# Kernel optimization log

Hardware: AMD Instinct MI355X
Metric: run time of the kernel (lower is better)

The kernel has to match this reference:

```python
import jax, jax.numpy as jnp
import numpy as np

B, T_ENC, T_DEC = 64, 512, 400
IN_DIM, R = 80, 2
D_ENC, D_ATT, D_PRE = 256, 256, 128
NEG_INF = -1e9


def _gru(x, h, Wi, Wh, bi, bh):
    # PyTorch GRUCell math
    gi = x @ Wi + bi
    gh = h @ Wh + bh
    ir, iz, inn = jnp.split(gi, 3, axis=-1)
    hr, hz, hn = jnp.split(gh, 3, axis=-1)
    r = jax.nn.sigmoid(ir + hr)
    z = jax.nn.sigmoid(iz + hz)
    n = jnp.tanh(inn + r * hn)
    return (1.0 - z) * n + z * h


def setup_inputs() -> dict:
    key = jax.random.key(0)
    ks = jax.random.split(key, 32)
    s = 0.05
    d_in = IN_DIM * R
    inp = {
        "encoder_outputs": jax.random.normal(ks[0], (B, T_ENC, D_ENC), jnp.float32),
        "inputs": jax.random.normal(ks[1], (B, T_DEC, d_in), jnp.float32),
        "memory_lengths": jax.random.randint(ks[2], (B,), T_ENC // 2, T_ENC + 1).astype(jnp.int32),
        # prenet
        "pre_W1": s * jax.random.normal(ks[3], (d_in, 256), jnp.float32),
        "pre_b1": jnp.zeros((256,), jnp.float32),
        "pre_W2": s * jax.random.normal(ks[4], (256, 128), jnp.float32),
        "pre_b2": jnp.zeros((128,), jnp.float32),
        # Bahdanau attention
        "mem_W": s * jax.random.normal(ks[5], (D_ENC, D_ATT), jnp.float32),
        "q_W": s * jax.random.normal(ks[6], (256, D_ATT), jnp.float32),
        "v_W": s * jax.random.normal(ks[7], (D_ATT, 1), jnp.float32),
        # attention GRUCell: input = cat(prenet 128, attention 256) = 384
        "att_Wi": s * jax.random.normal(ks[8], (384, 768), jnp.float32),
        "att_Wh": s * jax.random.normal(ks[9], (256, 768), jnp.float32),
        "att_bi": jnp.zeros((768,), jnp.float32),
        "att_bh": jnp.zeros((768,), jnp.float32),
        # project_to_decoder_in
        "proj_in_W": s * jax.random.normal(ks[10], (512, 256), jnp.float32),
        "proj_in_b": jnp.zeros((256,), jnp.float32),
        # decoder GRUCells
        "dec1_Wi": s * jax.random.normal(ks[11], (256, 768), jnp.float32),
        "dec1_Wh": s * jax.random.normal(ks[12], (256, 768), jnp.float32),
        "dec1_bi": jnp.zeros((768,), jnp.float32),
        "dec1_bh": jnp.zeros((768,), jnp.float32),
        "dec2_Wi": s * jax.random.normal(ks[13], (256, 768), jnp.float32),
        "dec2_Wh": s * jax.random.normal(ks[14], (256, 768), jnp.float32),
        "dec2_bi": jnp.zeros((768,), jnp.float32),
        "dec2_bh": jnp.zeros((768,), jnp.float32),
        # output projections
        "mel_W": s * jax.random.normal(ks[15], (256, d_in), jnp.float32),
        "mel_b": jnp.zeros((d_in,), jnp.float32),
        "gate_W": s * jax.random.normal(ks[16], (256, R), jnp.float32),
        "gate_b": jnp.zeros((R,), jnp.float32),
    }
    return inp


def _decoder_forward(encoder_outputs, inputs, memory_lengths,
                     pre_W1, pre_b1, pre_W2, pre_b2,
                     mem_W, q_W, v_W,
                     att_Wi, att_Wh, att_bi, att_bh,
                     proj_in_W, proj_in_b,
                     dec1_Wi, dec1_Wh, dec1_bi, dec1_bh,
                     dec2_Wi, dec2_Wh, dec2_bi, dec2_bh,
                     mel_W, mel_b, gate_W, gate_b):
    Bq, Tq, _ = encoder_outputs.shape
    processed_memory = encoder_outputs @ mem_W  # (B, T_enc, D_att)
    valid = jnp.arange(Tq)[None, :] < memory_lengths[:, None]  # (B, T_enc)

    # teacher forcing: input at step t is inputs[t-1], zeros at t=0
    prev = jnp.concatenate([jnp.zeros_like(inputs[:, :1]), inputs[:, :-1]], axis=1)
    prev = jnp.swapaxes(prev, 0, 1)  # (T_dec, B, in_dim*r)

    def prenet(x):
        # dropout is identity in eval mode
        h = jax.nn.relu(x @ pre_W1 + pre_b1)
        return jax.nn.relu(h @ pre_W2 + pre_b2)

    def step(carry, x_prev):
        att_h, h1, h2, cur_att = carry
        pre = prenet(x_prev)  # (B, 128)
        cell_in = jnp.concatenate([pre, cur_att], axis=-1)  # (B, 384)
        att_h = _gru(cell_in, att_h, att_Wi, att_Wh, att_bi, att_bh)  # (B, 256)
        # Bahdanau alignment over encoder memory
        score = jnp.squeeze(
            jnp.tanh(processed_memory + (att_h @ q_W)[:, None, :]) @ v_W, -1)  # (B, T_enc)
        score = jnp.where(valid, score, NEG_INF)
        align = jax.nn.softmax(score, axis=-1)
        cur_att = jnp.einsum('bt,btd->bd', align, encoder_outputs)  # (B, 256)
        dec_in = jnp.concatenate([att_h, cur_att], axis=-1) @ proj_in_W + proj_in_b
        h1 = _gru(dec_in, h1, dec1_Wi, dec1_Wh, dec1_bi, dec1_bh)
        d = h1 + dec_in
        h2 = _gru(d, h2, dec2_Wi, dec2_Wh, dec2_bi, dec2_bh)
        d = h2 + d
        gate = jax.nn.sigmoid(d @ gate_W + gate_b)  # (B, r)
        out = d @ mel_W + mel_b  # (B, in_dim*r)
        return (att_h, h1, h2, cur_att), (out, align, gate)

    z = jnp.zeros((Bq, 256), encoder_outputs.dtype)
    init = (z, z, z, z)
    _, (outs, aligns, gates) = jax.lax.scan(step, init, prev)
    outputs = jnp.swapaxes(outs, 0, 1)      # (B, T_dec, in_dim*r)
    alignments = jnp.swapaxes(aligns, 0, 1)  # (B, T_dec, T_enc)
    gates = jnp.swapaxes(gates, 0, 1)        # (B, T_dec, r)
    return outputs, alignments, gates


def reference(encoder_outputs, inputs, memory_lengths,
              pre_W1, pre_b1, pre_W2, pre_b2,
              mem_W, q_W, v_W,
              att_Wi, att_Wh, att_bi, att_bh,
              proj_in_W, proj_in_b,
              dec1_Wi, dec1_Wh, dec1_bi, dec1_bh,
              dec2_Wi, dec2_Wh, dec2_bi, dec2_bh,
              mel_W, mel_b, gate_W, gate_b):
    return _decoder_forward(encoder_outputs, inputs, memory_lengths,
                            pre_W1, pre_b1, pre_W2, pre_b2,
                            mem_W, q_W, v_W,
                            att_Wi, att_Wh, att_bi, att_bh,
                            proj_in_W, proj_in_b,
                            dec1_Wi, dec1_Wh, dec1_bi, dec1_bh,
                            dec2_Wi, dec2_Wh, dec2_bi, dec2_bh,
                            mel_W, mel_b, gate_W, gate_b)
```

## Files before the change

kernel.cpp:

```cpp
#include <hip/hip_runtime.h>

#define TDEC 400
#define NTH 512
#define NWG 256

typedef float f32x4 __attribute__((ext_vector_type(4)));
typedef unsigned u32x4 __attribute__((ext_vector_type(4)));
typedef unsigned u32x2 __attribute__((ext_vector_type(2)));

#define OFF_BAR   0
#define OFF_ATTH  11264
#define OFF_H1    44032
#define OFF_H2    76800
#define OFF_CURP  109568
#define OFF_ATTS  125952
#define OFF_Q     126208
#define ZERO_FLOATS 142592
#define OFF_D1    142592
#define OFF_SUMS  158976
#define OFF_C1    184576
#define OFF_PRE   185600
#define OFF_PMB   1824000
#define OFF_ENCB  6018304
#define OFF_D2A   10212608
#define T_WIT_A   10212608
#define T_WHT_A   10507520
#define T_M1T     10704128
#define T_WHT1    11097344
#define T_PJT     11293952
#define T_WIT2    11425024
#define T_WHT2    11621632
#define T_QWT     11818240
#define T_M1      11883776
#define OFF_BLOB  16766208

#define BLOB_N   26112
#define BLOB_STR 26624
#define BO_AI  0
#define BO_AH  4608
#define BO_Q   7680
#define BO_M1  8704
#define BO_H1  14848
#define BO_PJ  17920
#define BO_I2  19968
#define BO_H2  23040

#define AOFF 4096000
#define GOFF 17203200

#define MSTI  (8*1024)
#define GENI  (9*1024)
#define FAILI (10*1024)

__device__ __forceinline__ float fsig(float x){ return 1.0f/(1.0f+__expf(-x)); }
__device__ __forceinline__ float ftanh(float x){ float e = __expf(2.0f*x); return 1.0f - 2.0f/(e+1.0f); }
__device__ __forceinline__ float blo(unsigned u){ return __uint_as_float(u<<16); }
__device__ __forceinline__ float bhi(unsigned u){ return __uint_as_float(u & 0xffff0000u); }

__device__ __forceinline__ f32x4 cload16(const float* p){
  f32x4 r;
  asm volatile("global_load_dwordx4 %0, %1, off sc0 sc1" : "=v"(r) : "v"(p));
  return r;
}
__device__ __forceinline__ f32x4 cload16w(const float* p){
  f32x4 r;
  asm volatile("global_load_dwordx4 %0, %1, off sc0 sc1\n\ts_waitcnt vmcnt(0)" : "=v"(r) : "v"(p));
  return r;
}
__device__ __forceinline__ u32x4 cload16u(const unsigned short* p){
  u32x4 r;
  asm volatile("global_load_dwordx4 %0, %1, off sc0 sc1" : "=v"(r) : "v"(p));
  return r;
}
__device__ __forceinline__ float aload4(const float* p){
  unsigned u = __hip_atomic_load((const unsigned*)p, __ATOMIC_RELAXED, __HIP_MEMORY_SCOPE_AGENT);
  return __uint_as_float(u);
}
__device__ __forceinline__ void astore4(float* p, float v){
  __hip_atomic_store((unsigned*)p, __float_as_uint(v), __ATOMIC_RELAXED, __HIP_MEMORY_SCOPE_AGENT);
}
__device__ __forceinline__ void aadd(float* p, float v){
  __hip_atomic_fetch_add(p, v, __ATOMIC_RELAXED, __HIP_MEMORY_SCOPE_AGENT);
}
__device__ __forceinline__ int aloadi(const int* p){
  return __hip_atomic_load(p, __ATOMIC_RELAXED, __HIP_MEMORY_SCOPE_AGENT);
}

__device__ __forceinline__ void ldsbar(){
  __builtin_amdgcn_sched_barrier(0);
  asm volatile("s_waitcnt lgkmcnt(0)" ::: "memory");
  __builtin_amdgcn_s_barrier();
  __builtin_amdgcn_sched_barrier(0);
}

__device__ __forceinline__ void gbar(int* bar, int g, int l, int n){
  asm volatile("s_waitcnt vmcnt(0)" ::: "memory");
  __syncthreads();
  if (threadIdx.x == 0){
    if (aloadi(&bar[FAILI]) == 0){
      int a = __hip_atomic_fetch_add(&bar[(l&7)*1024 + g*64], 1, __ATOMIC_RELAXED, __HIP_MEMORY_SCOPE_AGENT);
      if (a == 8*n - 1){
        int m = __hip_atomic_fetch_add(&bar[MSTI + g*64], 1, __ATOMIC_RELAXED, __HIP_MEMORY_SCOPE_AGENT);
        if (m == 8*n - 1)
          __hip_atomic_store(&bar[GENI + g*64], n, __ATOMIC_RELAXED, __HIP_MEMORY_SCOPE_AGENT);
      }
      int sp = 0;
      while (aloadi(&bar[GENI + g*64]) < n){
        __builtin_amdgcn_s_sleep(1);
        if (++sp > (1<<20)){
          __hip_atomic_store(&bar[FAILI], 1, __ATOMIC_RELAXED, __HIP_MEMORY_SCOPE_AGENT);
          break;
        }
      }
    }
  }
  __syncthreads();
}

__device__ __forceinline__ unsigned short f2bf(float f){
  unsigned u = __float_as_uint(f);
  return (unsigned short)((u + 0x7fffu + ((u>>16)&1u)) >> 16);
}

template<int N8>
__device__ __forceinline__ float bdot(const unsigned short* wr, const float* xr){
  f32x4 accA = 0.f, accB = 0.f;
  #pragma unroll 4
  for (int k = 0; k < N8; ++k){
    u32x4 u = *(const u32x4*)(wr + k*8);
    f32x4 a = *(const f32x4*)(xr + k*8);
    f32x4 b = *(const f32x4*)(xr + k*8 + 4);
    f32x4 w0, w1;
    w0[0]=blo(u[0]); w0[1]=bhi(u[0]); w0[2]=blo(u[1]); w0[3]=bhi(u[1]);
    w1[0]=blo(u[2]); w1[1]=bhi(u[2]); w1[2]=blo(u[3]); w1[3]=bhi(u[3]);
    accA += w0*a; accB += w1*b;
  }
  f32x4 s = accA + accB;
  return s[0]+s[1]+s[2]+s[3];
}

__global__ __launch_bounds__(256, 1) void transpose_k(const float* __restrict__ in,
                                                      float* __restrict__ outp, int K, int C){
  __shared__ float tl[32][33];
  int c0 = blockIdx.x * 32, k0 = blockIdx.y * 32;
  int tx = threadIdx.x & 31, ty = threadIdx.x >> 5;
  for (int i = ty; i < 32; i += 8){
    int k = k0 + i, c = c0 + tx;
    if (k < K && c < C) tl[i][tx] = in[k * C + c];
  }
  __syncthreads();
  for (int i = ty; i < 32; i += 8){
    int c = c0 + i, k = k0 + tx;
    if (c < C && k < K) outp[c * K + k] = tl[tx][i];
  }
}

__global__ __launch_bounds__(128, 1) void fuse_k(const float* __restrict__ projW,
    const float* __restrict__ d1Wi, float* __restrict__ M1){
  int jt = blockIdx.x % 6, i = blockIdx.x / 6;
  int j = jt * 128 + threadIdx.x;
  float acc = 0.f;
  for (int k = 0; k < 256; ++k) acc += projW[i*256+k] * d1Wi[k*768+j];
  M1[i*768+j] = acc;
}

__global__ __launch_bounds__(256, 1) void c1_k(const float* __restrict__ projB,
    const float* __restrict__ d1Wi, const float* __restrict__ d1Bi, float* __restrict__ C1){
  int j = blockIdx.x * 256 + threadIdx.x;
  float acc = d1Bi[j];
  for (int k = 0; k < 256; ++k) acc += projB[k] * d1Wi[k*768+j];
  C1[j] = acc;
}

__global__ __launch_bounds__(512, 1) void pack_k(float* __restrict__ ws){
  int sl = blockIdx.x;
  const float* TAI = ws + T_WIT_A;
  const float* TAH = ws + T_WHT_A;
  const float* TM1 = ws + T_M1T;
  const float* TH1 = ws + T_WHT1;
  const float* TPJ = ws + T_PJT;
  const float* TI2 = ws + T_WIT2;
  const float* TH2 = ws + T_WHT2;
  const float* TQ  = ws + T_QWT;
  unsigned short* blob = (unsigned short*)(ws + OFF_BLOB) + (size_t)sl * BLOB_STR;
  for (int idx = threadIdx.x; idx < BLOB_N; idx += 512){
    float v; int cs, k, o;
    if (idx < BO_AH){ cs = idx / 384; k = idx - cs*384;
      v = TAI[((cs%3)*256 + sl*4 + cs/3)*384 + k]; }
    else if (idx < BO_Q){ o = idx - BO_AH; cs = o >> 8; k = o & 255;
      v = TAH[((cs%3)*256 + sl*4 + cs/3)*256 + k]; }
    else if (idx < BO_M1){ o = idx - BO_Q; cs = o >> 8; k = o & 255;
      v = TQ[(sl*4 + cs)*256 + k]; }
    else if (idx < BO_H1){ o = idx - BO_M1; cs = o >> 9; k = o & 511;
      v = TM1[((cs%3)*256 + sl*4 + cs/3)*512 + k]; }
    else if (idx < BO_PJ){ o = idx - BO_H1; cs = o >> 8; k = o & 255;
      v = TH1[((cs%3)*256 + sl*4 + cs/3)*256 + k]; }
    else if (idx < BO_I2){ o = idx - BO_PJ; cs = o >> 9; k = o & 511;
      v = TPJ[(sl*4 + cs)*512 + k]; }
    else if (idx < BO_H2){ o = idx - BO_I2; cs = o >> 8; k = o & 255;
      v = TI2[((cs%3)*256 + sl*4 + cs/3)*256 + k]; }
    else { o = idx - BO_H2; cs = o >> 8; k = o & 255;
      v = TH2[((cs%3)*256 + sl*4 + cs/3)*256 + k]; }
    blob[idx] = f2bf(v);
  }
}

__global__ __launch_bounds__(256, 1) void qt_k(const float* __restrict__ ws,
                                               float* __restrict__ out){
  unsigned short* qtb = (unsigned short*)(out + GOFF);
  const float* TQ = ws + T_QWT;
  int idx = blockIdx.x * 256 + threadIdx.x;
  int it = idx >> 11, j = (idx >> 3) & 255, e = idx & 7;
  qtb[idx] = f2bf(TQ[j*256 + it*8 + e]);
}

__global__ __launch_bounds__(NTH, 1) void prenet_k(float* __restrict__ ws,
    const float* __restrict__ inp, const float* __restrict__ W1, const float* __restrict__ B1,
    const float* __restrict__ W2, const float* __restrict__ B2){
  __shared__ float xT[160 * 33];
  __shared__ float hT[256 * 33];
  int t = blockIdx.x, half = blockIdx.y, tid = threadIdx.x;
  int bbase = half * 32;
  for (int r = tid; r < 32 * 160; r += NTH){
    int b2 = r / 160; int k = r - b2 * 160;
    xT[k * 33 + b2] = (t == 0) ? 0.f : inp[((bbase + b2) * TDEC + (t - 1)) * 160 + k];
  }
  __syncthreads();
  int bl = tid & 31, slot = tid >> 5;
  float acc1[16];
  #pragma unroll
  for (int i = 0; i < 16; ++i) acc1[i] = 0.f;
  for (int k = 0; k < 160; ++k){
    float xv = xT[k * 33 + bl];
    const float* wr = W1 + k * 256 + slot * 16;
    #pragma unroll
    for (int i = 0; i < 16; ++i) acc1[i] += xv * wr[i];
  }
  #pragma unroll
  for (int i = 0; i < 16; ++i){
    int c = slot * 16 + i;
    hT[c * 33 + bl] = fmaxf(acc1[i] + B1[c], 0.f);
  }
  __syncthreads();
  float acc2[8];
  #pragma unroll
  for (int i = 0; i < 8; ++i) acc2[i] = 0.f;
  for (int k = 0; k < 256; ++k){
    float hv = hT[k * 33 + bl];
    const float* wr = W2 + k * 128 + slot * 8;
    #pragma unroll
    for (int i = 0; i < 8; ++i) acc2[i] += hv * wr[i];
  }
  unsigned short* dst = (unsigned short*)(ws + OFF_PRE) + (size_t)t*8192 + (bbase + bl)*128 + slot*8;
  u32x4 pk;
  #pragma unroll
  for (int i = 0; i < 4; ++i){
    float v0 = fmaxf(acc2[2*i] + B2[slot*8 + 2*i], 0.f);
    float v1 = fmaxf(acc2[2*i+1] + B2[slot*8 + 2*i+1], 0.f);
    pk[i] = (unsigned)f2bf(v0) | ((unsigned)f2bf(v1) << 16);
  }
  *(u32x4*)dst = pk;
}

__global__ __launch_bounds__(NTH, 1) void pm_k(float* __restrict__ ws,
    const float* __restrict__ enc, const float* __restrict__ memW){
  int wg = blockIdx.x, tid = threadIdx.x;
  int b = wg & 63, th = wg >> 6;
  int slot = tid & 7, tt = tid >> 3;
  int trow = th * 64 + tt;
  const float* er = enc + ((size_t)(b * 512 + trow)) * 256;
  f32x4 acc[8];
  #pragma unroll
  for (int i = 0; i < 8; ++i) acc[i] = 0.f;
  for (int k = 0; k < 256; ++k){
    float ev = er[k];
    const f32x4* wr = (const f32x4*)(memW + k * 256 + slot * 32);
    #pragma unroll
    for (int i = 0; i < 8; ++i) acc[i] += ev * wr[i];
  }
  unsigned short* pmB = (unsigned short*)(ws + OFF_PMB);
  unsigned short* dst = pmB + ((size_t)(b * 512 + trow)) * 256 + slot * 32;
  #pragma unroll
  for (int i = 0; i < 8; ++i){
    u32x2 pk;
    pk[0] = (unsigned)f2bf(acc[i][0]) | ((unsigned)f2bf(acc[i][1]) << 16);
    pk[1] = (unsigned)f2bf(acc[i][2]) | ((unsigned)f2bf(acc[i][3]) << 16);
    *(u32x2*)(dst + i * 4) = pk;
  }
  const float* e2 = enc + ((size_t)(b * 512 + th * 64)) * 256;
  unsigned* eb = (unsigned*)((unsigned short*)(ws + OFF_ENCB) + ((size_t)(b * 512 + th * 64)) * 256);
  for (int i = tid; i < 64 * 128; i += NTH){
    float v0 = e2[i * 2], v1 = e2[i * 2 + 1];
    eb[i] = (unsigned)f2bf(v0) | ((unsigned)f2bf(v1) << 16);
  }
}

__global__ __launch_bounds__(NTH, 2) void decoder_k(
    float* __restrict__ ws, float* __restrict__ out,
    const int* __restrict__ memlen,
    const float* __restrict__ vW,
    const float* __restrict__ attBi, const float* __restrict__ attBh,
    const float* __restrict__ projB,
    const float* __restrict__ d1Bh,
    const float* __restrict__ d2Bi, const float* __restrict__ d2Bh)
{
  const int wg = blockIdx.x, tid = threadIdx.x;
  int* bar = (int*)ws;
  float* attH = ws + OFF_ATTH;
  float* h1a  = ws + OFF_H1;
  float* h2a  = ws + OFF_H2;
  float* const curB[2]  = { ws + OFF_CURP, ws + OFF_Q };
  float* const attSB[2] = { ws + OFF_ATTS, ws + OFF_ATTS + 64 };
  float* d1v  = ws + OFF_D1;
  const float* C1v = ws + OFF_C1;
  const unsigned short* preB16 = (const unsigned short*)(ws + OFF_PRE);
  const unsigned short* pmB  = (const unsigned short*)(ws + OFF_PMB);
  const unsigned short* encB = (const unsigned short*)(ws + OFF_ENCB);
  const unsigned short* qtb = (const unsigned short*)(out + GOFF);
  float* d2a  = ws + OFF_D2A;

  __shared__ float BUF[12416];
  __shared__ float qL[256], vL[256];
  __shared__ float eL[128];
  __shared__ float red[512];
  __shared__ float ewGi[192], ewGh[192], pdec[128];

  if (tid < 256) vL[tid] = vW[tid];

  const int g = wg >> 6, l = wg & 63;
  const int sl = l;
  const int b0 = g << 4;
  const int b2 = b0 + (l >> 2), ch2 = l & 3;
  const int len2 = memlen[b2];
  const unsigned short* blob = (const unsigned short*)(ws + OFF_BLOB) + (size_t)sl * BLOB_STR;

  const int bq = tid & 15, x = tid >> 4;
  const int cs = (x >= 12) ? (x - 12) : x;
  const int gg = cs % 3, jh = cs / 3;
  const int col = gg * 256 + sl * 4 + jh;

  const int r0 = tid >> 6, c0 = (tid & 63) << 2;
  const int r1 = r0 + 8;
  const int prr = tid >> 4, pcc = (tid & 15) * 8;

  u32x4 pmv[8], env[8];
  {
    int te = tid >> 2, part = tid & 3;
    const u32x4* pmp = (const u32x4*)(pmB + ((size_t)(b2*512 + ch2*128 + te))*256 + part*64);
    #pragma unroll
    for (int i = 0; i < 8; ++i) pmv[i] = pmp[i];
    int ich = tid >> 5, dblk = tid & 31;
    const unsigned short* ep = encB + ((size_t)(b2*512 + ch2*128 + ich*8))*256 + dblk*8;
    #pragma unroll
    for (int i = 0; i < 8; ++i) env[i] = *(const u32x4*)(ep + i*256);
  }

  f32x4 pH0, pH1, pC0, pC1;
  float pS0, pS1;
  u32x4 ppre = 0u;
  {
    const float* gHn = attH + 16384 + b0*256;
    const float* gCn = curB[1] + b0*256;
    pH0 = cload16(gHn + (r0<<8) + c0); pH1 = cload16(gHn + (r1<<8) + c0);
    pC0 = cload16(gCn + (r0<<8) + c0); pC1 = cload16(gCn + (r1<<8) + c0);
    pS0 = aload4(attSB[1] + b0 + r0);  pS1 = aload4(attSB[1] + b0 + r1);
    if (tid < 256) ppre = cload16u(preB16 + (b0 + prr)*128 + pcc);
  }

  int bn = 0;
  for (int t = 0; t < TDEC; ++t){
    const int w = t & 1, rb = w ^ 1;

    {
      float* xL = BUF;
      float* hL = BUF + 6208;
      asm volatile("s_waitcnt vmcnt(0)" : "+v"(pH0),"+v"(pH1),"+v"(pC0),"+v"(pC1),"+v"(ppre));
      float iv0 = pS0 > 0.f ? 1.f/pS0 : 0.f, iv1 = pS1 > 0.f ? 1.f/pS1 : 0.f;
      if (tid < 256){
        float* xd = xL + prr*388 + pcc;
        xd[0]=blo(ppre[0]); xd[1]=bhi(ppre[0]); xd[2]=blo(ppre[1]); xd[3]=bhi(ppre[1]);
        xd[4]=blo(ppre[2]); xd[5]=bhi(ppre[2]); xd[6]=blo(ppre[3]); xd[7]=bhi(ppre[3]);
      }
      *(f32x4*)(hL + r0*260 + c0) = pH0; *(f32x4*)(hL + r1*260 + c0) = pH1;
      *(f32x4*)(xL + r0*388 + 128 + c0) = pC0*iv0; *(f32x4*)(xL + r1*388 + 128 + c0) = pC1*iv1;
      if (tid < 64) astore4(curB[w] + wg*64 + tid, 0.f);
      if (sl == 0 && tid < 16) astore4(attSB[w] + b0 + tid, 0.f);
      ldsbar();
      if (x < 12)
        ewGi[cs*16 + bq] = bdot<48>(blob + BO_AI + cs*384, xL + bq*388) + attBi[col];
      else if (x < 24)
        ewGh[cs*16 + bq] = bdot<32>(blob + BO_AH + cs*256, hL + bq*260) + attBh[col];
      ldsbar();
      if (tid < 64){
        int bt = tid & 15, jj = tid >> 4;
        int j = sl*4 + jj;
        float ir = ewGi[(jj*3+0)*16+bt] + ewGh[(jj*3+0)*16+bt];
        float iz = ewGi[(jj*3+1)*16+bt] + ewGh[(jj*3+1)*16+bt];
        float inn = ewGi[(jj*3+2)*16+bt];
        float hn  = ewGh[(jj*3+2)*16+bt];
        float rg = fsig(ir), z = fsig(iz);
        float n = ftanh(inn + rg * hn);
        float h = hL[bt*260 + j];
        astore4(attH + w*16384 + (b0+bt)*256 + j, (1.f - z)*n + z*h);
      }
    }
    gbar(bar, g, l, ++bn);

    {
      float* ctxP = BUF;
      float* qIn  = BUF + 8192;
      if (tid < 64){
        f32x4 v = cload16w(attH + w*16384 + b2*256 + tid*4);
        *(f32x4*)(qIn + tid*4) = v;
      }
      ldsbar();
      {
        int j = tid & 255, hf = tid >> 8;
        const unsigned short* qw = qtb + j*8 + (size_t)hf*16*2048;
        const float* qx = qIn + hf*128;
        f32x4 aA = 0.f, aB = 0.f;
        #pragma unroll 4
        for (int it = 0; it < 16; ++it){
          u32x4 u = *(const u32x4*)(qw + (size_t)it*2048);
          f32x4 a = *(const f32x4*)(qx + it*8);
          f32x4 b = *(const f32x4*)(qx + it*8 + 4);
          f32x4 w0, w1;
          w0[0]=blo(u[0]); w0[1]=bhi(u[0]); w0[2]=blo(u[1]); w0[3]=bhi(u[1]);
          w1[0]=blo(u[2]); w1[1]=bhi(u[2]); w1[2]=blo(u[3]); w1[3]=bhi(u[3]);
          aA += w0*a; aB += w1*b;
        }
        f32x4 s4 = aA + aB;
        red[tid] = s4[0]+s4[1]+s4[2]+s4[3];
      }
      ldsbar();
      if (tid < 256) qL[tid] = red[tid] + red[tid + 256];
      ldsbar();
      {
        int te = tid >> 2, part = tid & 3;
        int ge = ch2*128 + te;
        float a4 = 0.f;
        #pragma unroll
        for (int i = 0; i < 8; ++i){
          u32x4 u = pmv[i];
          int kb = part*64 + i*8;
          a4 += ftanh(blo(u[0]) + qL[kb+0]) * vL[kb+0];
          a4 += ftanh(bhi(u[0]) + qL[kb+1]) * vL[kb+1];
          a4 += ftanh(blo(u[1]) + qL[kb+2]) * vL[kb+2];
          a4 += ftanh(bhi(u[1]) + qL[kb+3]) * vL[kb+3];
          a4 += ftanh(blo(u[2]) + qL[kb+4]) * vL[kb+4];
          a4 += ftanh(bhi(u[2]) + qL[kb+5]) * vL[kb+5];
          a4 += ftanh(blo(u[3]) + qL[kb+6]) * vL[kb+6];
          a4 += ftanh(bhi(u[3]) + qL[kb+7]) * vL[kb+7];
        }
        a4 += __shfl_xor(a4, 1);
        a4 += __shfl_xor(a4, 2);
        float e = (ge < len2) ? __expf(a4) : 0.f;
        if (part == 0){
          eL[te] = e;
          out[AOFF + ((size_t)(b2*TDEC + t))*512 + ge] = e;
        }
      }
      ldsbar();
      if (tid < 64){
        float s = eL[tid] + eL[tid + 64];
        #pragma unroll
        for (int o = 32; o > 0; o >>= 1) s += __shfl_down(s, o);
        if (tid == 0) aadd(attSB[w] + b2, s);
      }
      {
        int ich = tid >> 5, dblk = tid & 31;
        f32x4 acA = 0.f, acB = 0.f;
        #pragma unroll
        for (int i = 0; i < 8; ++i){
          u32x4 u = env[i];
          float e = eL[ich*8 + i];
          acA[0] += e*blo(u[0]); acA[1] += e*bhi(u[0]);
          acA[2] += e*blo(u[1]); acA[3] += e*bhi(u[1]);
          acB[0] += e*blo(u[2]); acB[1] += e*bhi(u[2]);
          acB[2] += e*blo(u[3]); acB[3] += e*bhi(u[3]);
        }
        *(f32x4*)(ctxP + tid*8) = acA;
        *(f32x4*)(ctxP + tid*8 + 4) = acB;
      }
      ldsbar();
      if (tid < 256){
        int dblk = tid >> 3, d = tid & 7;
        float s = 0.f;
        #pragma unroll
        for (int i = 0; i < 16; ++i) s += ctxP[i*256 + dblk*8 + d];
        aadd(curB[w] + b2*256 + dblk*8 + d, s);
      }
    }
    gbar(bar, g, l, ++bn);

    {
      float* yL  = BUF;
      float* h1L = BUF + 8256;
      const float* gA = attH + w*16384 + b0*256;
      const float* gH = h1a + rb*16384 + b0*256;
      const float* gC = curB[w] + b0*256;
      f32x4 vA0 = cload16(gA + (r0<<8) + c0), vA1 = cload16(gA + (r1<<8) + c0);
      f32x4 vH0 = cload16(gH + (r0<<8) + c0), vH1 = cload16(gH + (r1<<8) + c0);
      f32x4 vC0 = cload16(gC + (r0<<8) + c0), vC1 = cload16(gC + (r1<<8) + c0);
      float s0 = aload4(attSB[w] + b0 + r0), s1 = aload4(attSB[w] + b0 + r1);
      asm volatile("s_waitcnt vmcnt(0)" : "+v"(vA0),"+v"(vA1),"+v"(vH0),"+v"(vH1),"+v"(vC0),"+v"(vC1));
      float iv0 = s0 > 0.f ? 1.f/s0 : 0.f, iv1 = s1 > 0.f ? 1.f/s1 : 0.f;
      *(f32x4*)(yL + r0*516 + c0) = vA0;       *(f32x4*)(yL + r1*516 + c0) = vA1;
      *(f32x4*)(h1L + r0*260 + c0) = vH0;      *(f32x4*)(h1L + r1*260 + c0) = vH1;
      *(f32x4*)(yL + r0*516 + 256 + c0) = vC0*iv0; *(f32x4*)(yL + r1*516 + 256 + c0) = vC1*iv1;
      ldsbar();
      if (x < 12)
        ewGi[cs*16 + bq] = bdot<64>(blob + BO_M1 + cs*512, yL + bq*516) + C1v[col];
      else if (x < 24)
        ewGh[cs*16 + bq] = bdot<32>(blob + BO_H1 + cs*256, h1L + bq*260) + d1Bh[col];
      else {
        int idx = tid - 384;
        int bq2 = idx & 15, cc = (idx >> 4) & 3, half = idx >> 6;
        pdec[idx] = bdot<32>(blob + BO_PJ + cc*512 + half*256, yL + bq2*516 + half*256);
      }
      ldsbar();
      if (tid < 64){
        int bt = tid & 15, jj = tid >> 4;
        int j = sl*4 + jj;
        float ir = ewGi[(jj*3+0)*16+bt] + ewGh[(jj*3+0)*16+bt];
        float iz = ewGi[(jj*3+1)*16+bt] + ewGh[(jj*3+1)*16+bt];
        float inn = ewGi[(jj*3+2)*16+bt];
        float hn  = ewGh[(jj*3+2)*16+bt];
        float rg = fsig(ir), z = fsig(iz);
        float n = ftanh(inn + rg * hn);
        float hv = h1L[bt*260 + j];
        float hnew = (1.f - z)*n + z*hv;
        float dec = pdec[jj*16 + bt] + pdec[64 + jj*16 + bt] + projB[j];
        astore4(h1a + w*16384 + (b0+bt)*256 + j, hnew);
        astore4(d1v + (b0+bt)*256 + j, hnew + dec);
      }
      if (sl == 0 && tid < 16)
        ws[OFF_SUMS + t*64 + b0 + tid] = aload4(attSB[w] + b0 + tid);
    }
    gbar(bar, g, l, ++bn);

    {
      float* dL  = BUF;
      float* h2L = BUF + 4160;
      const float* gD = d1v + b0*256;
      const float* gH = h2a + rb*16384 + b0*256;
      f32x4 vD0 = cload16(gD + (r0<<8) + c0), vD1 = cload16(gD + (r1<<8) + c0);
      f32x4 vH0 = cload16(gH + (r0<<8) + c0), vH1 = cload16(gH + (r1<<8) + c0);
      asm volatile("s_waitcnt vmcnt(0)" : "+v"(vD0),"+v"(vD1),"+v"(vH0),"+v"(vH1));
      {
        const float* gHn = attH + w*16384 + b0*256;
        const float* gCn = curB[w] + b0*256;
        pH0 = cload16(gHn + (r0<<8) + c0); pH1 = cload16(gHn + (r1<<8) + c0);
        pC0 = cload16(gCn + (r0<<8) + c0); pC1 = cload16(gCn + (r1<<8) + c0);
        pS0 = aload4(attSB[w] + b0 + r0);  pS1 = aload4(attSB[w] + b0 + r1);
        int tn = (t + 1 < TDEC) ? (t + 1) : 0;
        if (tid < 256) ppre = cload16u(preB16 + (size_t)tn*8192 + (b0 + prr)*128 + pcc);
      }
      *(f32x4*)(dL + r0*260 + c0) = vD0;  *(f32x4*)(dL + r1*260 + c0) = vD1;
      *(f32x4*)(h2L + r0*260 + c0) = vH0; *(f32x4*)(h2L + r1*260 + c0) = vH1;
      ldsbar();
      if (x < 12)
        ewGi[cs*16 + bq] = bdot<32>(blob + BO_I2 + cs*256, dL + bq*260) + d2Bi[col];
      else if (x < 24)
        ewGh[cs*16 + bq] = bdot<32>(blob + BO_H2 + cs*256, h2L + bq*260) + d2Bh[col];
      ldsbar();
      if (tid < 64){
        int bt = tid & 15, jj = tid >> 4;
        int j = sl*4 + jj;
        float ir = ewGi[(jj*3+0)*16+bt] + ewGh[(jj*3+0)*16+bt];
        float iz = ewGi[(jj*3+1)*16+bt] + ewGh[(jj*3+1)*16+bt];
        float inn = ewGi[(jj*3+2)*16+bt];
        float hn  = ewGh[(jj*3+2)*16+bt];
        float rg = fsig(ir), z = fsig(iz);
        float n = ftanh(inn + rg * hn);
        float hv = h2L[bt*260 + j];
        float hnew = (1.f - z)*n + z*hv;
        astore4(h2a + w*16384 + (b0+bt)*256 + j, hnew);
        d2a[t*16384 + j*64 + (b0+bt)] = hnew + dL[bt*260 + j];
      }
      ldsbar();
    }
  }
}

__global__ __launch_bounds__(NTH, 1) void rescale_k(const float* __restrict__ ws,
                                                    float* __restrict__ out){
  int blk = blockIdx.x;
  int b = blk / TDEC, t = blk - b * TDEC;
  float s = ws[OFF_SUMS + t*64 + b];
  float inv = (s > 0.f) ? 1.f/s : 0.f;
  out[AOFF + (size_t)blk*512 + threadIdx.x] *= inv;
}

__global__ __launch_bounds__(NTH, 1) void outproj_k(const float* __restrict__ ws,
    float* __restrict__ out, const float* __restrict__ melW, const float* __restrict__ melB,
    const float* __restrict__ gateW, const float* __restrict__ gateB){
  int t = blockIdx.x, tid = threadIdx.x;
  int cx = tid & 255, bh = tid >> 8;
  const float* src = ws + OFF_D2A + t*16384 + bh*32;
  float acc[32];
  #pragma unroll
  for (int i = 0; i < 32; ++i) acc[i] = 0.f;
  bool ismel = (cx < 160);
  bool isgate = (cx >= 160 && cx < 162);
  for (int j = 0; j < 256; ++j){
    float wv = 0.f;
    if (ismel) wv = melW[j*160 + cx];
    else if (isgate) wv = gateW[j*2 + (cx - 160)];
    const f32x4* dp = (const f32x4*)(src + j*64);
    f32x4 vv[8];
    #pragma unroll
    for (int q = 0; q < 8; ++q) vv[q] = dp[q];
    #pragma unroll
    for (int q = 0; q < 8; ++q){
      acc[q*4+0] += vv[q][0]*wv; acc[q*4+1] += vv[q][1]*wv;
      acc[q*4+2] += vv[q][2]*wv; acc[q*4+3] += vv[q][3]*wv;
    }
  }
  if (ismel){
    float bb = melB[cx];
    #pragma unroll
    for (int i = 0; i < 32; ++i){
      int b = bh*32 + i;
      out[((size_t)(b*TDEC + t))*160 + cx] = acc[i] + bb;
    }
  } else if (isgate){
    int g = cx - 160;
    float bb = gateB[g];
    #pragma unroll
    for (int i = 0; i < 32; ++i){
      int b = bh*32 + i;
      out[GOFF + ((size_t)(b*TDEC + t))*2 + g] = fsig(acc[i] + bb);
    }
  }
}

extern "C" void kernel_launch(void* const* d_in, const int* in_sizes, int n_in,
                              void* d_out, int out_size, void* d_ws, size_t ws_size,
                              hipStream_t stream)
{
  (void)in_sizes; (void)n_in; (void)out_size; (void)ws_size;
  const float* enc   = (const float*)d_in[0];
  const float* inp   = (const float*)d_in[1];
  const int*   mlen  = (const int*)d_in[2];
  const float* preW1 = (const float*)d_in[3];
  const float* preB1 = (const float*)d_in[4];
  const float* preW2 = (const float*)d_in[5];
  const float* preB2 = (const float*)d_in[6];
  const float* memW  = (const float*)d_in[7];
  const float* qW    = (const float*)d_in[8];
  const float* vW    = (const float*)d_in[9];
  const float* attWi = (const float*)d_in[10];
  const float* attWh = (const float*)d_in[11];
  const float* attBi = (const float*)d_in[12];
  const float* attBh = (const float*)d_in[13];
  const float* projW = (const float*)d_in[14];
  const float* projB = (const float*)d_in[15];
  const float* d1Wi  = (const float*)d_in[16];
  const float* d1Wh  = (const float*)d_in[17];
  const float* d1Bi  = (const float*)d_in[18];
  const float* d1Bh  = (const float*)d_in[19];
  const float* d2Wi  = (const float*)d_in[20];
  const float* d2Wh  = (const float*)d_in[21];
  const float* d2Bi  = (const float*)d_in[22];
  const float* d2Bh  = (const float*)d_in[23];
  const float* melW  = (const float*)d_in[24];
  const float* melB  = (const float*)d_in[25];
  const float* gateW = (const float*)d_in[26];
  const float* gateB = (const float*)d_in[27];
  float* ws = (float*)d_ws;
  float* out = (float*)d_out;

  hipMemsetAsync(d_ws, 0, (size_t)ZERO_FLOATS * sizeof(float), stream);

  dim3 tt(256);
  transpose_k<<<dim3(24, 12), tt, 0, stream>>>(attWi, ws + T_WIT_A, 384, 768);
  transpose_k<<<dim3(24, 8),  tt, 0, stream>>>(attWh, ws + T_WHT_A, 256, 768);
  transpose_k<<<dim3(24, 8),  tt, 0, stream>>>(d1Wh,  ws + T_WHT1, 256, 768);
  transpose_k<<<dim3(24, 8),  tt, 0, stream>>>(d2Wi,  ws + T_WIT2, 256, 768);
  transpose_k<<<dim3(24, 8),  tt, 0, stream>>>(d2Wh,  ws + T_WHT2, 256, 768);
  transpose_k<<<dim3(8, 16),  tt, 0, stream>>>(projW, ws + T_PJT, 512, 256);
  transpose_k<<<dim3(8, 8),   tt, 0, stream>>>(qW,    ws + T_QWT, 256, 256);
  fuse_k<<<3072, 128, 0, stream>>>(projW, d1Wi, ws + T_M1);
  c1_k<<<3, 256, 0, stream>>>(projB, d1Wi, d1Bi, ws + OFF_C1);
  transpose_k<<<dim3(24, 16), tt, 0, stream>>>(ws + T_M1, ws + T_M1T, 512, 768);
  pack_k<<<64, NTH, 0, stream>>>(ws);
  qt_k<<<256, 256, 0, stream>>>(ws, out);

  prenet_k<<<dim3(TDEC, 2), NTH, 0, stream>>>(ws, inp, preW1, preB1, preW2, preB2);
  pm_k<<<512, NTH, 0, stream>>>(ws, enc, memW);
  decoder_k<<<NWG, NTH, 0, stream>>>(ws, out, mlen, vW, attBi, attBh, projB,
                                     d1Bh, d2Bi, d2Bh);
  rescale_k<<<64 * TDEC, NTH, 0, stream>>>(ws, out);
  outproj_k<<<TDEC, NTH, 0, stream>>>(ws, out, melW, melB, gateW, gateB);
}
```

Baseline: 13.32 ms.

## Double workgroup count to 512 with 8-batch groups and split-K GRU dots

Grows the persistent decoder grid from 256 to 512 workgroups, so each group of 64 workgroups handles 8 batch rows instead of 16 and each attention chunk covers 64 encoder positions instead of 128. The GRU gate dot products are split across two K halves and combined with a lane shuffle, and GRU biases are hoisted into registers before the time loop. The aim is to shorten the per-step serial work between the grid barriers and use more CUs. In exchange the grid barriers span more workgroups, and the query projection and per-step global loads are duplicated across more workgroups.

```diff
diff --git a/kernel.cpp b/kernel.cpp
--- a/kernel.cpp
+++ b/kernel.cpp
@@ -2,7 +2,7 @@
 
 #define TDEC 400
 #define NTH 512
-#define NWG 256
+#define NWG 512
 
 typedef float f32x4 __attribute__((ext_vector_type(4)));
 typedef unsigned u32x4 __attribute__((ext_vector_type(4)));
@@ -319,52 +319,56 @@
   const unsigned short* qtb = (const unsigned short*)(out + GOFF);
   float* d2a  = ws + OFF_D2A;
 
-  __shared__ float BUF[12416];
+  __shared__ float BUF[6208];
   __shared__ float qL[256], vL[256];
-  __shared__ float eL[128];
-  __shared__ float red[512];
-  __shared__ float ewGi[192], ewGh[192], pdec[128];
+  __shared__ float eL[64];
+  __shared__ float ewGi[96], ewGh[96], pdec[32];
 
   if (tid < 256) vL[tid] = vW[tid];
 
   const int g = wg >> 6, l = wg & 63;
   const int sl = l;
-  const int b0 = g << 4;
-  const int b2 = b0 + (l >> 2), ch2 = l & 3;
+  const int b0 = g << 3;
+  const int b2 = b0 + (l >> 3), ch2 = l & 7;
   const int len2 = memlen[b2];
   const unsigned short* blob = (const unsigned short*)(ws + OFF_BLOB) + (size_t)sl * BLOB_STR;
 
-  const int bq = tid & 15, x = tid >> 4;
-  const int cs = (x >= 12) ? (x - 12) : x;
-  const int gg = cs % 3, jh = cs / 3;
-  const int col = gg * 256 + sl * 4 + jh;
-
+  const int bq = tid & 7, x = tid >> 3;
   const int r0 = tid >> 6, c0 = (tid & 63) << 2;
-  const int r1 = r0 + 8;
   const int prr = tid >> 4, pcc = (tid & 15) * 8;
 
-  u32x4 pmv[8], env[8];
+  int cs = 0, kh = 0;
+  if (x < 24){ cs = x >> 1; kh = x & 1; }
+  else if (x < 48){ cs = (x - 24) >> 1; kh = x & 1; }
+  float rb0 = 0.f, rb1 = 0.f, rb2 = 0.f;
+  if (x < 48 && kh == 0){
+    int gg2 = cs % 3, jh2 = cs / 3;
+    int col = gg2*256 + sl*4 + jh2;
+    if (x < 24){ rb0 = attBi[col]; rb1 = C1v[col];  rb2 = d2Bi[col]; }
+    else       { rb0 = attBh[col]; rb1 = d1Bh[col]; rb2 = d2Bh[col]; }
+  }
+  const float pjB = (tid < 32) ? projB[sl*4 + (tid>>3)] : 0.f;
+
+  u32x4 pmv[4]; u32x2 env2[8];
   {
-    int te = tid >> 2, part = tid & 3;
-    const u32x4* pmp = (const u32x4*)(pmB + ((size_t)(b2*512 + ch2*128 + te))*256 + part*64);
-    #pragma unroll
-    for (int i = 0; i < 8; ++i) pmv[i] = pmp[i];
-    int ich = tid >> 5, dblk = tid & 31;
-    const unsigned short* ep = encB + ((size_t)(b2*512 + ch2*128 + ich*8))*256 + dblk*8;
-    #pragma unroll
-    for (int i = 0; i < 8; ++i) env[i] = *(const u32x4*)(ep + i*256);
-  }
-
-  f32x4 pH0, pH1, pC0, pC1;
-  float pS0, pS1;
+    int te = tid >> 3, part = tid & 7;
+    const u32x4* pmp = (const u32x4*)(pmB + ((size_t)(b2*512 + ch2*64 + te))*256 + part*32);
+    #pragma unroll
+    for (int i = 0; i < 4; ++i) pmv[i] = pmp[i];
+    int ich = tid >> 6, dd = tid & 63;
+    const unsigned short* ep = encB + ((size_t)(b2*512 + ch2*64 + ich*8))*256 + dd*4;
+    #pragma unroll
+    for (int i = 0; i < 8; ++i) env2[i] = *(const u32x2*)(ep + i*256);
+  }
+
+  f32x4 pH, pC;
+  float pS;
   u32x4 ppre = 0u;
   {
-    const float* gHn = attH + 16384 + b0*256;
-    const float* gCn = curB[1] + b0*256;
-    pH0 = cload16(gHn + (r0<<8) + c0); pH1 = cload16(gHn + (r1<<8) + c0);
-    pC0 = cload16(gCn + (r0<<8) + c0); pC1 = cload16(gCn + (r1<<8) + c0);
-    pS0 = aload4(attSB[1] + b0 + r0);  pS1 = aload4(attSB[1] + b0 + r1);
-    if (tid < 256) ppre = cload16u(preB16 + (b0 + prr)*128 + pcc);
+    pH = cload16(attH + 16384 + (b0+r0)*256 + c0);
+    pC = cload16(curB[1] + (b0+r0)*256 + c0);
+    pS = aload4(attSB[1] + b0 + r0);
+    if (tid < 128) ppre = cload16u(preB16 + (b0 + prr)*128 + pcc);
   }
 
   int bn = 0;
@@ -373,31 +377,36 @@
 
     {
       float* xL = BUF;
-      float* hL = BUF + 6208;
-      asm volatile("s_waitcnt vmcnt(0)" : "+v"(pH0),"+v"(pH1),"+v"(pC0),"+v"(pC1),"+v"(ppre));
-      float iv0 = pS0 > 0.f ? 1.f/pS0 : 0.f, iv1 = pS1 > 0.f ? 1.f/pS1 : 0.f;
-      if (tid < 256){
+      float* hL = BUF + 3104;
+      asm volatile("s_waitcnt vmcnt(0)" : "+v"(pH),"+v"(pC),"+v"(ppre));
+      float iv = pS > 0.f ? 1.f/pS : 0.f;
+      if (tid < 128){
         float* xd = xL + prr*388 + pcc;
         xd[0]=blo(ppre[0]); xd[1]=bhi(ppre[0]); xd[2]=blo(ppre[1]); xd[3]=bhi(ppre[1]);
         xd[4]=blo(ppre[2]); xd[5]=bhi(ppre[2]); xd[6]=blo(ppre[3]); xd[7]=bhi(ppre[3]);
       }
-      *(f32x4*)(hL + r0*260 + c0) = pH0; *(f32x4*)(hL + r1*260 + c0) = pH1;
-      *(f32x4*)(xL + r0*388 + 128 + c0) = pC0*iv0; *(f32x4*)(xL + r1*388 + 128 + c0) = pC1*iv1;
-      if (tid < 64) astore4(curB[w] + wg*64 + tid, 0.f);
-      if (sl == 0 && tid < 16) astore4(attSB[w] + b0 + tid, 0.f);
-      ldsbar();
-      if (x < 12)
-        ewGi[cs*16 + bq] = bdot<48>(blob + BO_AI + cs*384, xL + bq*388) + attBi[col];
-      else if (x < 24)
-        ewGh[cs*16 + bq] = bdot<32>(blob + BO_AH + cs*256, hL + bq*260) + attBh[col];
-      ldsbar();
-      if (tid < 64){
-        int bt = tid & 15, jj = tid >> 4;
+      *(f32x4*)(hL + r0*260 + c0) = pH;
+      *(f32x4*)(xL + r0*388 + 128 + c0) = pC*iv;
+      if (tid < 32) astore4(curB[w] + wg*32 + tid, 0.f);
+      if (l == 0 && tid < 8) astore4(attSB[w] + b0 + tid, 0.f);
+      ldsbar();
+      {
+        float acc = 0.f;
+        if (x < 24)       acc = bdot<24>(blob + BO_AI + cs*384 + kh*192, xL + bq*388 + kh*192);
+        else if (x < 48)  acc = bdot<16>(blob + BO_AH + cs*256 + kh*128, hL + bq*260 + kh*128);
+        if (x < 48){
+          acc += __shfl_xor(acc, 8);
+          if (kh == 0) (x < 24 ? ewGi : ewGh)[cs*8 + bq] = acc + rb0;
+        }
+      }
+      ldsbar();
+      if (tid < 32){
+        int bt = tid & 7, jj = tid >> 3;
         int j = sl*4 + jj;
-        float ir = ewGi[(jj*3+0)*16+bt] + ewGh[(jj*3+0)*16+bt];
-        float iz = ewGi[(jj*3+1)*16+bt] + ewGh[(jj*3+1)*16+bt];
-        float inn = ewGi[(jj*3+2)*16+bt];
-        float hn  = ewGh[(jj*3+2)*16+bt];
+        float ir = ewGi[(jj*3+0)*8+bt] + ewGh[(jj*3+0)*8+bt];
+        float iz = ewGi[(jj*3+1)*8+bt] + ewGh[(jj*3+1)*8+bt];
+        float inn = ewGi[(jj*3+2)*8+bt];
+        float hn  = ewGh[(jj*3+2)*8+bt];
         float rg = fsig(ir), z = fsig(iz);
         float n = ftanh(inn + rg * hn);
         float h = hL[bt*260 + j];
@@ -408,41 +417,37 @@
 
     {
       float* ctxP = BUF;
-      float* qIn  = BUF + 8192;
+      float* qIn  = BUF + 2560;
       if (tid < 64){
         f32x4 v = cload16w(attH + w*16384 + b2*256 + tid*4);
         *(f32x4*)(qIn + tid*4) = v;
       }
       ldsbar();
-      {
-        int j = tid & 255, hf = tid >> 8;
-        const unsigned short* qw = qtb + j*8 + (size_t)hf*16*2048;
-        const float* qx = qIn + hf*128;
+      if (tid < 256){
+        const unsigned short* qw = qtb + tid*8;
         f32x4 aA = 0.f, aB = 0.f;
         #pragma unroll 4
-        for (int it = 0; it < 16; ++it){
+        for (int it = 0; it < 32; ++it){
           u32x4 u = *(const u32x4*)(qw + (size_t)it*2048);
-          f32x4 a = *(const f32x4*)(qx + it*8);
-          f32x4 b = *(const f32x4*)(qx + it*8 + 4);
+          f32x4 a = *(const f32x4*)(qIn + it*8);
+          f32x4 b = *(const f32x4*)(qIn + it*8 + 4);
           f32x4 w0, w1;
           w0[0]=blo(u[0]); w0[1]=bhi(u[0]); w0[2]=blo(u[1]); w0[3]=bhi(u[1]);
           w1[0]=blo(u[2]); w1[1]=bhi(u[2]); w1[2]=blo(u[3]); w1[3]=bhi(u[3]);
           aA += w0*a; aB += w1*b;
         }
         f32x4 s4 = aA + aB;
-        red[tid] = s4[0]+s4[1]+s4[2]+s4[3];
-      }
-      ldsbar();
-      if (tid < 256) qL[tid] = red[tid] + red[tid + 256];
+        qL[tid] = s4[0]+s4[1]+s4[2]+s4[3];
+      }
       ldsbar();
       {
-        int te = tid >> 2, part = tid & 3;
-        int ge = ch2*128 + te;
+        int te = tid >> 3, part = tid & 7;
+        int ge = ch2*64 + te;
         float a4 = 0.f;
         #pragma unroll
-        for (int i = 0; i < 8; ++i){
+        for (int i = 0; i < 4; ++i){
           u32x4 u = pmv[i];
-          int kb = part*64 + i*8;
+          int kb = part*32 + i*8;
           a4 += ftanh(blo(u[0]) + qL[kb+0]) * vL[kb+0];
           a4 += ftanh(bhi(u[0]) + qL[kb+1]) * vL[kb+1];
           a4 += ftanh(blo(u[1]) + qL[kb+2]) * vL[kb+2];
@@ -454,6 +459,7 @@
         }
         a4 += __shfl_xor(a4, 1);
         a4 += __shfl_xor(a4, 2);
+        a4 += __shfl_xor(a4, 4);
         float e = (ge < len2) ? __expf(a4) : 0.f;
         if (part == 0){
           eL[te] = e;
@@ -462,115 +468,116 @@
       }
       ldsbar();
       if (tid < 64){
-        float s = eL[tid] + eL[tid + 64];
+        float s = eL[tid];
         #pragma unroll
         for (int o = 32; o > 0; o >>= 1) s += __shfl_down(s, o);
         if (tid == 0) aadd(attSB[w] + b2, s);
       }
       {
-        int ich = tid >> 5, dblk = tid & 31;
-        f32x4 acA = 0.f, acB = 0.f;
+        int ich = tid >> 6, dd = tid & 63;
+        f32x4 ac = 0.f;
         #pragma unroll
         for (int i = 0; i < 8; ++i){
-          u32x4 u = env[i];
+          u32x2 u = env2[i];
           float e = eL[ich*8 + i];
-          acA[0] += e*blo(u[0]); acA[1] += e*bhi(u[0]);
-          acA[2] += e*blo(u[1]); acA[3] += e*bhi(u[1]);
-          acB[0] += e*blo(u[2]); acB[1] += e*bhi(u[2]);
-          acB[2] += e*blo(u[3]); acB[3] += e*bhi(u[3]);
-        }
-        *(f32x4*)(ctxP + tid*8) = acA;
-        *(f32x4*)(ctxP + tid*8 + 4) = acB;
+          ac[0] += e*blo(u[0]); ac[1] += e*bhi(u[0]);
+          ac[2] += e*blo(u[1]); ac[3] += e*bhi(u[1]);
+        }
+        *(f32x4*)(ctxP + ich*256 + dd*4) = ac;
       }
       ldsbar();
       if (tid < 256){
-        int dblk = tid >> 3, d = tid & 7;
         float s = 0.f;
         #pragma unroll
-        for (int i = 0; i < 16; ++i) s += ctxP[i*256 + dblk*8 + d];
-        aadd(curB[w] + b2*256 + dblk*8 + d, s);
+        for (int i = 0; i < 8; ++i) s += ctxP[i*256 + tid];
+        aadd(curB[w] + b2*256 + tid, s);
       }
     }
     gbar(bar, g, l, ++bn);
 
     {
       float* yL  = BUF;
-      float* h1L = BUF + 8256;
-      const float* gA = attH + w*16384 + b0*256;
-      const float* gH = h1a + rb*16384 + b0*256;
-      const float* gC = curB[w] + b0*256;
-      f32x4 vA0 = cload16(gA + (r0<<8) + c0), vA1 = cload16(gA + (r1<<8) + c0);
-      f32x4 vH0 = cload16(gH + (r0<<8) + c0), vH1 = cload16(gH + (r1<<8) + c0);
-      f32x4 vC0 = cload16(gC + (r0<<8) + c0), vC1 = cload16(gC + (r1<<8) + c0);
-      float s0 = aload4(attSB[w] + b0 + r0), s1 = aload4(attSB[w] + b0 + r1);
-      asm volatile("s_waitcnt vmcnt(0)" : "+v"(vA0),"+v"(vA1),"+v"(vH0),"+v"(vH1),"+v"(vC0),"+v"(vC1));
-      float iv0 = s0 > 0.f ? 1.f/s0 : 0.f, iv1 = s1 > 0.f ? 1.f/s1 : 0.f;
-      *(f32x4*)(yL + r0*516 + c0) = vA0;       *(f32x4*)(yL + r1*516 + c0) = vA1;
-      *(f32x4*)(h1L + r0*260 + c0) = vH0;      *(f32x4*)(h1L + r1*260 + c0) = vH1;
-      *(f32x4*)(yL + r0*516 + 256 + c0) = vC0*iv0; *(f32x4*)(yL + r1*516 + 256 + c0) = vC1*iv1;
-      ldsbar();
-      if (x < 12)
-        ewGi[cs*16 + bq] = bdot<64>(blob + BO_M1 + cs*512, yL + bq*516) + C1v[col];
-      else if (x < 24)
-        ewGh[cs*16 + bq] = bdot<32>(blob + BO_H1 + cs*256, h1L + bq*260) + d1Bh[col];
-      else {
-        int idx = tid - 384;
-        int bq2 = idx & 15, cc = (idx >> 4) & 3, half = idx >> 6;
-        pdec[idx] = bdot<32>(blob + BO_PJ + cc*512 + half*256, yL + bq2*516 + half*256);
-      }
-      ldsbar();
-      if (tid < 64){
-        int bt = tid & 15, jj = tid >> 4;
+      float* h1L = BUF + 4128;
+      f32x4 vA = cload16(attH + w*16384 + (b0+r0)*256 + c0);
+      f32x4 vH = cload16(h1a + rb*16384 + (b0+r0)*256 + c0);
+      f32x4 vC = cload16(curB[w] + (b0+r0)*256 + c0);
+      float s0 = aload4(attSB[w] + b0 + r0);
+      asm volatile("s_waitcnt vmcnt(0)" : "+v"(vA),"+v"(vH),"+v"(vC));
+      float iv = s0 > 0.f ? 1.f/s0 : 0.f;
+      *(f32x4*)(yL + r0*516 + c0) = vA;
+      *(f32x4*)(h1L + r0*260 + c0) = vH;
+      *(f32x4*)(yL + r0*516 + 256 + c0) = vC*iv;
+      ldsbar();
+      {
+        float acc = 0.f;
+        if (x < 24)       acc = bdot<32>(blob + BO_M1 + cs*512 + kh*256, yL + bq*516 + kh*256);
+        else if (x < 48)  acc = bdot<16>(blob + BO_H1 + cs*256 + kh*128, h1L + bq*260 + kh*128);
+        else {
+          int idx = x - 48, cc = idx >> 2, qq = idx & 3;
+          acc = bdot<16>(blob + BO_PJ + cc*512 + qq*128, yL + bq*516 + qq*128);
+          acc += __shfl_xor(acc, 8);
+          acc += __shfl_xor(acc, 16);
+          if (qq == 0) pdec[cc*8 + bq] = acc;
+        }
+        if (x < 48){
+          acc += __shfl_xor(acc, 8);
+          if (kh == 0) (x < 24 ? ewGi : ewGh)[cs*8 + bq] = acc + rb1;
+        }
+      }
+      ldsbar();
+      if (tid < 32){
+        int bt = tid & 7, jj = tid >> 3;
         int j = sl*4 + jj;
-        float ir = ewGi[(jj*3+0)*16+bt] + ewGh[(jj*3+0)*16+bt];
-        float iz = ewGi[(jj*3+1)*16+bt] + ewGh[(jj*3+1)*16+bt];
-        float inn = ewGi[(jj*3+2)*16+bt];
-        float hn  = ewGh[(jj*3+2)*16+bt];
+        float ir = ewGi[(jj*3+0)*8+bt] + ewGh[(jj*3+0)*8+bt];
+        float iz = ewGi[(jj*3+1)*8+bt] + ewGh[(jj*3+1)*8+bt];
+        float inn = ewGi[(jj*3+2)*8+bt];
+        float hn  = ewGh[(jj*3+2)*8+bt];
         float rg = fsig(ir), z = fsig(iz);
         float n = ftanh(inn + rg * hn);
         float hv = h1L[bt*260 + j];
         float hnew = (1.f - z)*n + z*hv;
-        float dec = pdec[jj*16 + bt] + pdec[64 + jj*16 + bt] + projB[j];
+        float dec = pdec[jj*8 + bt] + pjB;
         astore4(h1a + w*16384 + (b0+bt)*256 + j, hnew);
         astore4(d1v + (b0+bt)*256 + j, hnew + dec);
       }
-      if (sl == 0 && tid < 16)
+      if (l == 0 && tid < 8)
         ws[OFF_SUMS + t*64 + b0 + tid] = aload4(attSB[w] + b0 + tid);
     }
     gbar(bar, g, l, ++bn);
 
     {
       float* dL  = BUF;
-      float* h2L = BUF + 4160;
-      const float* gD = d1v + b0*256;
-      const float* gH = h2a + rb*16384 + b0*256;
-      f32x4 vD0 = cload16(gD + (r0<<8) + c0), vD1 = cload16(gD + (r1<<8) + c0);
-      f32x4 vH0 = cload16(gH + (r0<<8) + c0), vH1 = cload16(gH + (r1<<8) + c0);
-      asm volatile("s_waitcnt vmcnt(0)" : "+v"(vD0),"+v"(vD1),"+v"(vH0),"+v"(vH1));
+      float* h2L = BUF + 2080;
+      f32x4 vD = cload16(d1v + (b0+r0)*256 + c0);
+      f32x4 vH = cload16(h2a + rb*16384 + (b0+r0)*256 + c0);
+      asm volatile("s_waitcnt vmcnt(0)" : "+v"(vD),"+v"(vH));
       {
-        const float* gHn = attH + w*16384 + b0*256;
-        const float* gCn = curB[w] + b0*256;
-        pH0 = cload16(gHn + (r0<<8) + c0); pH1 = cload16(gHn + (r1<<8) + c0);
-        pC0 = cload16(gCn + (r0<<8) + c0); pC1 = cload16(gCn + (r1<<8) + c0);
-        pS0 = aload4(attSB[w] + b0 + r0);  pS1 = aload4(attSB[w] + b0 + r1);
+        pH = cload16(attH + w*16384 + (b0+r0)*256 + c0);
+        pC = cload16(curB[w] + (b0+r0)*256 + c0);
+        pS = aload4(attSB[w] + b0 + r0);
         int tn = (t + 1 < TDEC) ? (t + 1) : 0;
-        if (tid < 256) ppre = cload16u(preB16 + (size_t)tn*8192 + (b0 + prr)*128 + pcc);
-      }
-      *(f32x4*)(dL + r0*260 + c0) = vD0;  *(f32x4*)(dL + r1*260 + c0) = vD1;
-      *(f32x4*)(h2L + r0*260 + c0) = vH0; *(f32x4*)(h2L + r1*260 + c0) = vH1;
-      ldsbar();
-      if (x < 12)
-        ewGi[cs*16 + bq] = bdot<32>(blob + BO_I2 + cs*256, dL + bq*260) + d2Bi[col];
-      else if (x < 24)
-        ewGh[cs*16 + bq] = bdot<32>(blob + BO_H2 + cs*256, h2L + bq*260) + d2Bh[col];
-      ldsbar();
-      if (tid < 64){
-        int bt = tid & 15, jj = tid >> 4;
+        if (tid < 128) ppre = cload16u(preB16 + (size_t)tn*8192 + (b0 + prr)*128 + pcc);
+      }
+      *(f32x4*)(dL + r0*260 + c0) = vD;
+      *(f32x4*)(h2L + r0*260 + c0) = vH;
+      ldsbar();
+      {
+        float acc = 0.f;
+        if (x < 24)       acc = bdot<16>(blob + BO_I2 + cs*256 + kh*128, dL + bq*260 + kh*128);
+        else if (x < 48)  acc = bdot<16>(blob + BO_H2 + cs*256 + kh*128, h2L + bq*260 + kh*128);
+        if (x < 48){
+          acc += __shfl_xor(acc, 8);
+          if (kh == 0) (x < 24 ? ewGi : ewGh)[cs*8 + bq] = acc + rb2;
+        }
+      }
+      ldsbar();
+      if (tid < 32){
+        int bt = tid & 7, jj = tid >> 3;
         int j = sl*4 + jj;
-        float ir = ewGi[(jj*3+0)*16+bt] + ewGh[(jj*3+0)*16+bt];
-        float iz = ewGi[(jj*3+1)*16+bt] + ewGh[(jj*3+1)*16+bt];
-        float inn = ewGi[(jj*3+2)*16+bt];
-        float hn  = ewGh[(jj*3+2)*16+bt];
+        float ir = ewGi[(jj*3+0)*8+bt] + ewGh[(jj*3+0)*8+bt];
+        float iz = ewGi[(jj*3+1)*8+bt] + ewGh[(jj*3+1)*8+bt];
+        float inn = ewGi[(jj*3+2)*8+bt];
+        float hn  = ewGh[(jj*3+2)*8+bt];
         float rg = fsig(ir), z = fsig(iz);
         float n = ftanh(inn + rg * hn);
         float hv = h2L[bt*260 + j];
```

After: 17.26 ms. 1.3x slower.
